# Kernel optimization log

Measured on AMD Instinct MI355X. Metric: run time of the kernel, lower is better.

## Reference

```python
import jax, jax.numpy as jnp
import numpy as np

L = 2048          # seq len
DIM = 1024        # model dim
NL = 12           # num layers
VOCAB = 50257
PAD_VOCAB = 50264 # vocab padded to multiple of 8 for embedding
N = 16            # ssm state dim
K = 4             # conv kernel size
E = 2048          # d_inner = expand * dim
DTR = 64          # dt_rank = ceil(dim/16)
EPS = 1e-5


def setup_inputs() -> dict:
    key = jax.random.key(0)
    ks = jax.random.split(key, 12)
    s = 0.02
    f32 = jnp.float32
    # HiPPO-style A init: A_log = log(1..N) broadcast over channels
    A_log = jnp.log(jnp.broadcast_to(jnp.arange(1, N + 1, dtype=f32), (NL, E, N)))
    return {
        "input_ids": jax.random.randint(ks[0], (L,), 0, VOCAB),
        "embed": jax.random.normal(ks[1], (PAD_VOCAB, DIM), f32) * s,
        "in_proj_w": jax.random.normal(ks[2], (NL, 2 * E, DIM), f32) * s,
        "conv_w": jax.random.normal(ks[3], (NL, E, K), f32) * s,
        "conv_b": jnp.zeros((NL, E), f32),
        "x_proj_w": jax.random.normal(ks[4], (NL, DTR + 2 * N, E), f32) * s,
        "dt_proj_w": jax.random.normal(ks[5], (NL, E, DTR), f32) * s,
        "dt_proj_b": jax.random.normal(ks[6], (NL, E), f32) * 0.1,
        "A_log": A_log,
        "D_param": jnp.ones((NL, E), f32),
        "out_proj_w": jax.random.normal(ks[7], (NL, DIM, E), f32) * s,
        "norm_w": jnp.ones((NL, DIM), f32),
        "norm_f_w": jnp.ones((DIM,), f32),
        "head_w": jax.random.normal(ks[8], (VOCAB, DIM), f32) * s,
    }


def rmsnorm(x, w):
    # per-token RMSNorm over last axis (matches eqx.nn.RMSNorm vmapped per token)
    inv = jax.lax.rsqrt(jnp.mean(x * x, axis=-1, keepdims=True) + EPS)
    return x * inv * w


def causal_dw_conv(x, w, b):
    # x: [L, E], w: [E, K] depthwise causal conv, b: [E]
    out = jax.lax.conv_general_dilated(
        x.T[None],            # [1, E, L]
        w[:, None, :],        # [E, 1, K]
        (1,), [(K - 1, 0)],
        feature_group_count=E,
        dimension_numbers=("NCH", "OIH", "NCH"),
    )
    return out[0].T + b       # [L, E]


def mamba_block(x, in_w, cw, cb, xp_w, dt_w, dt_b, A_log, D, out_w):
    # x: [L, DIM]
    xz = x @ in_w.T                       # [L, 2E]
    xi, z = xz[:, :E], xz[:, E:]
    xc = jax.nn.silu(causal_dw_conv(xi, cw, cb))   # [L, E]
    dbc = xc @ xp_w.T                     # [L, DTR + 2N]
    dt = jax.nn.softplus(dbc[:, :DTR] @ dt_w.T + dt_b)  # [L, E]
    B = dbc[:, DTR:DTR + N]               # [L, N]
    C = dbc[:, DTR + N:]                  # [L, N]
    A = -jnp.exp(A_log)                   # [E, N]
    dA = jnp.exp(dt[:, :, None] * A)                       # [L, E, N]
    dBu = dt[:, :, None] * B[:, None, :] * xc[:, :, None]  # [L, E, N]

    def step(h, inp):
        dA_t, dBu_t = inp
        h = dA_t * h + dBu_t
        return h, h

    _, hs = jax.lax.scan(step, jnp.zeros((E, N), x.dtype), (dA, dBu))
    y = jnp.einsum("len,ln->le", hs, C) + D * xc
    y = y * jax.nn.silu(z)
    return y @ out_w.T                    # [L, DIM]


def reference(input_ids, embed, in_proj_w, conv_w, conv_b, x_proj_w,
              dt_proj_w, dt_proj_b, A_log, D_param, out_proj_w,
              norm_w, norm_f_w, head_w):
    x = embed[input_ids]                  # [L, DIM]
    res = None
    for i in range(NL):
        res = x + res if res is not None else x
        h = rmsnorm(res, norm_w[i])
        x = mamba_block(h, in_proj_w[i], conv_w[i], conv_b[i], x_proj_w[i],
                        dt_proj_w[i], dt_proj_b[i], A_log[i], D_param[i],
                        out_proj_w[i])
    res = x + res
    x = rmsnorm(res, norm_f_w)
    return x @ head_w.T                   # [L, VOCAB]
```

## Files before the change

### kernel.cpp

```cpp
#include <hip/hip_runtime.h>
#include <math.h>

#define LSEQ 2048
#define DMODEL 1024
#define NLAYER 12
#define NVOCAB 50257
#define NPADV 50304
#define EDIM 2048
#define NST 16
#define DTRANK 64
#define EPSV 1e-5f
#define NCHUNK 64
#define TCHUNK 32

typedef __attribute__((ext_vector_type(4))) float float4v;
typedef __attribute__((ext_vector_type(8))) short short8v;
typedef __attribute__((ext_vector_type(4))) unsigned short ushort4v;
typedef unsigned short u16;

__device__ __forceinline__ u16 f2bf(float f) {
    union { float f; unsigned int u; } v; v.f = f;
    unsigned int r = v.u + 0x7FFFu + ((v.u >> 16) & 1u);
    return (u16)(r >> 16);
}

__device__ __forceinline__ ushort4v cvt4(float4 a) {
    ushort4v r; r[0] = f2bf(a.x); r[1] = f2bf(a.y); r[2] = f2bf(a.z); r[3] = f2bf(a.w);
    return r;
}

__device__ __forceinline__ float4v mfma_bf16(short8v a, short8v b, float4v c) {
    return __builtin_amdgcn_mfma_f32_16x16x32_bf16(a, b, c, 0, 0, 0);
}

__device__ __forceinline__ void gload_lds16(const void* g, void* l) {
    __builtin_amdgcn_global_load_lds(
        (const __attribute__((address_space(1))) unsigned int*)g,
        (__attribute__((address_space(3))) unsigned int*)l,
        16, 0, 0);
}

__global__ __launch_bounds__(256) void k_embed(const int* __restrict__ ids,
                                               const float* __restrict__ emb,
                                               float* __restrict__ res) {
    const int t = blockIdx.x;
    const int row = ids[t];
    ((float4*)(res + (size_t)t * DMODEL))[threadIdx.x] =
        ((const float4*)(emb + (size_t)row * DMODEL))[threadIdx.x];
}

template<bool ADD>
__global__ __launch_bounds__(256) void k_addnorm(float* __restrict__ res,
                                                 const float* __restrict__ xin,
                                                 const float* __restrict__ w,
                                                 u16* __restrict__ h) {
    const int t = blockIdx.x;
    const int i = threadIdx.x;
    float4 r = ((float4*)(res + (size_t)t * DMODEL))[i];
    if (ADD) {
        float4 xv = ((const float4*)(xin + (size_t)t * DMODEL))[i];
        r.x += xv.x; r.y += xv.y; r.z += xv.z; r.w += xv.w;
        ((float4*)(res + (size_t)t * DMODEL))[i] = r;
    }
    float ss = r.x * r.x + r.y * r.y + r.z * r.z + r.w * r.w;
#pragma unroll
    for (int off = 32; off > 0; off >>= 1) ss += __shfl_xor(ss, off);
    __shared__ float part[4];
    if ((i & 63) == 0) part[i >> 6] = ss;
    __syncthreads();
    float tot = part[0] + part[1] + part[2] + part[3];
    const float inv = rsqrtf(tot * (1.f / DMODEL) + EPSV);
    float4 wv = ((const float4*)w)[i];
    float4 o;
    o.x = r.x * inv * wv.x; o.y = r.y * inv * wv.y;
    o.z = r.z * inv * wv.z; o.w = r.w * inv * wv.w;
    ((ushort4v*)(h + (size_t)t * DMODEL))[i] = cvt4(o);
}

__global__ __launch_bounds__(256) void k_cvt(const float* __restrict__ s, u16* __restrict__ d,
                                             long long n, long long ntot) {
    const long long stride = (long long)gridDim.x * 256 * 8;
    for (long long i = ((long long)blockIdx.x * 256 + threadIdx.x) * 8; i < ntot; i += stride) {
        ushort4v lo, hi;
        if (i < n) {
            float4 a = *(const float4*)(s + i);
            float4 b = *(const float4*)(s + i + 4);
            lo = cvt4(a); hi = cvt4(b);
        } else {
            lo[0] = lo[1] = lo[2] = lo[3] = 0;
            hi[0] = hi[1] = hi[2] = hi[3] = 0;
        }
        *(ushort4v*)(d + i) = lo;
        *(ushort4v*)(d + i + 4) = hi;
    }
}

__global__ __launch_bounds__(256) void k_cvtL(const float* __restrict__ sa, u16* __restrict__ da, long long na,
                                              const float* __restrict__ sb, u16* __restrict__ db, long long nb,
                                              const float* __restrict__ sc, u16* __restrict__ dc, long long nc,
                                              const float* __restrict__ sd, u16* __restrict__ dd, long long nd) {
    const long long tot = na + nb + nc + nd;
    const long long stride = (long long)gridDim.x * 256 * 8;
    for (long long i = ((long long)blockIdx.x * 256 + threadIdx.x) * 8; i < tot; i += stride) {
        const float* s; u16* d; long long o = i;
        if (o < na) { s = sa; d = da; }
        else { o -= na;
            if (o < nb) { s = sb; d = db; }
            else { o -= nb;
                if (o < nc) { s = sc; d = dc; }
                else { o -= nc; s = sd; d = dd; } } }
        float4 a = *(const float4*)(s + o);
        float4 b = *(const float4*)(s + o + 4);
        *(ushort4v*)(d + o) = cvt4(a);
        *(ushort4v*)(d + o + 4) = cvt4(b);
    }
}

template<int MT, int EPI, bool NTS>
__global__ __launch_bounds__(256, 3) void k_gemm128(const u16* __restrict__ A,
                                                    const u16* __restrict__ W,
                                                    float* __restrict__ C,
                                                    const float* __restrict__ bias,
                                                    int N, int K, int ldc, int cpx) {
    __shared__ __align__(128) u16 lds[3][8192];
    const int tid = threadIdx.x;
    const int w = tid >> 6;
    const int lane = tid & 63;
    const int l16 = lane & 15;
    const int quad = lane >> 4;
    const int wm = (w >> 1) * 64;
    const int wn = (w & 1) * 64;
    const int bid = blockIdx.x;
    const int orig = (bid & 7) * cpx + (bid >> 3);
    const int bm = orig & (MT - 1);
    const int bn = orig / MT;
    const int row0 = bm * 128, col0 = bn * 128;

    const int scol = ((lane & 3) ^ ((lane >> 3) & 3)) * 8;
    const int lrow = lane >> 2;
    const u16* sbase[4];
#pragma unroll
    for (int c = 0; c < 4; ++c) {
        const int g = w * 4 + c;
        sbase[c] = (g < 8 ? A + (size_t)(row0 + g * 16 + lrow) * K
                          : W + (size_t)(col0 + (g - 8) * 16 + lrow) * K) + scol;
    }

    const int swz = (quad ^ ((l16 >> 1) & 3)) * 8;
    const int aoff = (wm + l16) * 32 + swz;
    const int boff = 4096 + (wn + l16) * 32 + swz;

    float4v acc[4][4];
#pragma unroll
    for (int i = 0; i < 4; ++i)
#pragma unroll
        for (int j = 0; j < 4; ++j)
#pragma unroll
            for (int r = 0; r < 4; ++r) acc[i][j][r] = 0.f;

    const int NT = K >> 5;
    u16* lds0 = &lds[0][0];

    auto stage_tile = [&](int buf, int t) {
        u16* dst = lds0 + buf * 8192;
#pragma unroll
        for (int c = 0; c < 4; ++c)
            gload_lds16(sbase[c] + t * 32, dst + (w * 4 + c) * 512);
    };

    stage_tile(0, 0);
    stage_tile(1, 1);
    asm volatile("s_waitcnt vmcnt(4)" ::: "memory");
    __builtin_amdgcn_s_barrier();

    int cur = 0;
    for (int n = 0; n < NT; ++n) {
        const u16* Ls = lds0 + cur * 8192;
        short8v af[4], bf[4];
#pragma unroll
        for (int ii = 0; ii < 4; ++ii)
            af[ii] = *(const short8v*)&Ls[aoff + ii * 512];
#pragma unroll
        for (int j = 0; j < 4; ++j)
            bf[j] = *(const short8v*)&Ls[boff + j * 512];
        const bool pf = (n + 2 < NT);
        if (pf) {
            int tg = cur + 2; if (tg >= 3) tg -= 3;
            stage_tile(tg, n + 2);
        }
        __builtin_amdgcn_s_setprio(1);
#pragma unroll
        for (int ii = 0; ii < 4; ++ii)
#pragma unroll
            for (int j = 0; j < 4; ++j)
                acc[ii][j] = mfma_bf16(af[ii], bf[j], acc[ii][j]);
        __builtin_amdgcn_s_setprio(0);
        if (pf)
            asm volatile("s_waitcnt vmcnt(4)" ::: "memory");
        else if (n + 1 < NT)
            asm volatile("s_waitcnt vmcnt(0)" ::: "memory");
        __builtin_amdgcn_s_barrier();
        ++cur; if (cur == 3) cur = 0;
    }

    float* lt = (float*)lds0 + (size_t)w * 1040;
    const int ecol = col0 + wn + lane;
    float bv = 0.f;
    if (EPI == 1) bv = bias[(ecol < N) ? ecol : 0];
#pragma unroll
    for (int i = 0; i < 4; ++i) {
        __syncthreads();
#pragma unroll
        for (int j = 0; j < 4; ++j)
#pragma unroll
            for (int r = 0; r < 4; ++r)
                lt[(quad * 4 + r) * 65 + j * 16 + l16] = acc[i][j][r];
        __syncthreads();
        if (ecol < N) {
            const int rbase = row0 + wm + i * 16;
#pragma unroll
            for (int t = 0; t < 16; ++t) {
                float v = lt[t * 65 + lane];
                if (EPI == 1) { v += bv; v = (v > 20.f) ? v : log1pf(__expf(v)); }
                float* p = &C[(size_t)(rbase + t) * ldc + ecol];
                if (NTS) __builtin_nontemporal_store(v, p);
                else *p = v;
            }
        }
    }
}

template<int MT>
__global__ __launch_bounds__(256, 3) void k_gemm64(const u16* __restrict__ A,
                                                   const u16* __restrict__ W,
                                                   float* __restrict__ C,
                                                   int N, int K, int ldc, int cpx) {
    __shared__ __align__(128) u16 lds[3][8192];
    const int tid = threadIdx.x;
    const int w = tid >> 6;
    const int lane = tid & 63;
    const int l16 = lane & 15;
    const int quad = lane >> 4;
    const int wm = (w >> 1) * 32;
    const int wn = (w & 1) * 32;
    const int bid = blockIdx.x;
    const int orig = (bid & 7) * cpx + (bid >> 3);
    const int bm = orig & (MT - 1);
    const int bn = orig / MT;
    const int row0 = bm * 64, col0 = bn * 64;

    const int scol = ((lane & 3) ^ ((lane >> 3) & 3)) * 8;
    const int lrow = lane >> 2;
    const u16* sbase[4];
#pragma unroll
    for (int c = 0; c < 4; ++c) {
        const int ch = w * 4 + c;
        const int isA = (ch < 8);
        const int cc = isA ? ch : (ch - 8);
        const int half = cc >> 2;
        const int rbase = (cc & 3) * 16;
        sbase[c] = (isA ? A + (size_t)(row0 + rbase + lrow) * K
                        : W + (size_t)(col0 + rbase + lrow) * K) + half * 32 + scol;
    }

    const int swz = (quad ^ ((l16 >> 1) & 3)) * 8;
    const int aoff = (wm + l16) * 32 + swz;
    const int boff = 4096 + (wn + l16) * 32 + swz;

    float4v acc[2][2];
#pragma unroll
    for (int i = 0; i < 2; ++i)
#pragma unroll
        for (int j = 0; j < 2; ++j)
#pragma unroll
            for (int r = 0; r < 4; ++r) acc[i][j][r] = 0.f;

    const int NT = K >> 6;
    u16* lds0 = &lds[0][0];

    auto stage_tile = [&](int buf, int t) {
        u16* dst = lds0 + buf * 8192;
#pragma unroll
        for (int c = 0; c < 4; ++c)
            gload_lds16(sbase[c] + t * 64, dst + (w * 4 + c) * 512);
    };

    stage_tile(0, 0);
    stage_tile(1, 1);
    asm volatile("s_waitcnt vmcnt(4)" ::: "memory");
    __builtin_amdgcn_s_barrier();

    int cur = 0;
    for (int n = 0; n < NT; ++n) {
        const u16* Ls = lds0 + cur * 8192;
        short8v af[2][2], bf[2][2];
#pragma unroll
        for (int ks = 0; ks < 2; ++ks) {
#pragma unroll
            for (int ii = 0; ii < 2; ++ii)
                af[ks][ii] = *(const short8v*)&Ls[ks * 2048 + aoff + ii * 512];
#pragma unroll
            for (int j = 0; j < 2; ++j)
                bf[ks][j] = *(const short8v*)&Ls[ks * 2048 + boff + j * 512];
        }
        const bool pf = (n + 2 < NT);
        if (pf) {
            int tg = cur + 2; if (tg >= 3) tg -= 3;
            stage_tile(tg, n + 2);
        }
        __builtin_amdgcn_s_setprio(1);
#pragma unroll
        for (int ks = 0; ks < 2; ++ks)
#pragma unroll
            for (int ii = 0; ii < 2; ++ii)
#pragma unroll
                for (int j = 0; j < 2; ++j)
                    acc[ii][j] = mfma_bf16(af[ks][ii], bf[ks][j], acc[ii][j]);
        __builtin_amdgcn_s_setprio(0);
        if (pf)
            asm volatile("s_waitcnt vmcnt(4)" ::: "memory");
        else if (n + 1 < NT)
            asm volatile("s_waitcnt vmcnt(0)" ::: "memory");
        __builtin_amdgcn_s_barrier();
        ++cur; if (cur == 3) cur = 0;
    }

    float* lt = (float*)lds0 + (size_t)w * 528;
    const int c32 = lane & 31;
    const int rsub = lane >> 5;
    const int ecol = col0 + wn + c32;
#pragma unroll
    for (int i = 0; i < 2; ++i) {
        __syncthreads();
#pragma unroll
        for (int j = 0; j < 2; ++j)
#pragma unroll
            for (int r = 0; r < 4; ++r)
                lt[(quad * 4 + r) * 33 + j * 16 + l16] = acc[i][j][r];
        __syncthreads();
        if (ecol < N) {
            const int rbase = row0 + wm + i * 16;
#pragma unroll
            for (int t = 0; t < 8; ++t)
                C[(size_t)(rbase + 2 * t + rsub) * ldc + ecol] =
                    lt[(2 * t + rsub) * 33 + c32];
        }
    }
}

__global__ __launch_bounds__(256) void k_conv(const float* __restrict__ xz,
                                              const float* __restrict__ cw,
                                              const float* __restrict__ cb,
                                              float* __restrict__ xc,
                                              u16* __restrict__ xc16) {
    const int e = blockIdx.x * 256 + threadIdx.x;
    const int t0 = blockIdx.y * 8;
    const float w0 = cw[e * 4 + 0], w1 = cw[e * 4 + 1], w2 = cw[e * 4 + 2], w3 = cw[e * 4 + 3];
    const float b = cb[e];
    float xm3 = (t0 >= 3) ? xz[(size_t)(t0 - 3) * (2 * EDIM) + e] : 0.f;
    float xm2 = (t0 >= 2) ? xz[(size_t)(t0 - 2) * (2 * EDIM) + e] : 0.f;
    float xm1 = (t0 >= 1) ? xz[(size_t)(t0 - 1) * (2 * EDIM) + e] : 0.f;
#pragma unroll
    for (int s = 0; s < 8; ++s) {
        const int t = t0 + s;
        const float xt = xz[(size_t)t * (2 * EDIM) + e];
        const float v = w0 * xm3 + w1 * xm2 + w2 * xm1 + w3 * xt + b;
        const float sv = v / (1.f + __expf(-v));
        xc[(size_t)t * EDIM + e] = sv;
        xc16[(size_t)t * EDIM + e] = f2bf(sv);
        xm3 = xm2; xm2 = xm1; xm1 = xt;
    }
}

__global__ __launch_bounds__(256) void k_xproj(const u16* __restrict__ xc,
                                               const u16* __restrict__ W,
                                               float* __restrict__ dbc,
                                               u16* __restrict__ dbc16) {
    const int tid = threadIdx.x;
    const int wave = tid >> 6, lane = tid & 63;
    const int l16 = lane & 15, quad = lane >> 4;
    const int m = blockIdx.x * 16 + l16;
    const int kb = wave * (EDIM / 4);
    float4v acc[6];
#pragma unroll
    for (int j = 0; j < 6; ++j)
#pragma unroll
        for (int r = 0; r < 4; ++r) acc[j][r] = 0.f;

    for (int ks = 0; ks < EDIM / 4; ks += 32) {
        const int k = kb + ks + quad * 8;
        const short8v af = *(const short8v*)(xc + (size_t)m * EDIM + k);
#pragma unroll
        for (int j = 0; j < 6; ++j) {
            const short8v bf = *(const short8v*)(W + (size_t)(j * 16 + l16) * EDIM + k);
            acc[j] = mfma_bf16(af, bf, acc[j]);
        }
    }
    __shared__ float red[4][16][96];
#pragma unroll
    for (int j = 0; j < 6; ++j)
#pragma unroll
        for (int r = 0; r < 4; ++r)
            red[wave][quad * 4 + r][j * 16 + l16] = acc[j][r];
    __syncthreads();
    for (int idx = tid; idx < 16 * 96; idx += 256) {
        const int r = idx / 96, c = idx % 96;
        const float s = red[0][r][c] + red[1][r][c] + red[2][r][c] + red[3][r][c];
        const int row = blockIdx.x * 16 + r;
        dbc[(size_t)row * 96 + c] = s;
        if (c < 64) dbc16[(size_t)row * 64 + c] = f2bf(s);
    }
}

__global__ __launch_bounds__(256) void k_scanA(const float* __restrict__ dt,
                                               const float* __restrict__ xc,
                                               const float* __restrict__ dbc,
                                               const float* __restrict__ Al,
                                               float* __restrict__ hpart,
                                               float* __restrict__ sdtb) {
    const int e = blockIdx.y * 256 + threadIdx.x;
    const int c = blockIdx.x;
    float a[NST];
#pragma unroll
    for (int n = 0; n < NST; ++n) a[n] = -__expf(Al[(size_t)e * NST + n]);
    bool fast = true;
#pragma unroll
    for (int n = 0; n < NST; ++n)
        fast = fast && (fabsf(a[n] + (float)(n + 1)) < 1e-3f * (float)(n + 1));
    __align__(16) float h[NST];
#pragma unroll
    for (int n = 0; n < NST; ++n) h[n] = 0.f;
    float sdt = 0.f;
    const int t0 = c * TCHUNK;
    if (fast) {
        for (int s = 0; s < TCHUNK; ++s) {
            const int t = t0 + s;
            const float d = dt[(size_t)t * EDIM + e];
            const float x = xc[(size_t)t * EDIM + e];
            __align__(16) float Bv[NST];
#pragma unroll
            for (int q = 0; q < 4; ++q)
                *(float4*)&Bv[q * 4] = *(const float4*)&dbc[(size_t)t * 96 + 64 + q * 4];
            const float u = d * x;
            sdt += d;
            const float d1 = __expf(-d);
            float pw = 1.f;
#pragma unroll
            for (int n = 0; n < NST; ++n) { pw *= d1; h[n] = fmaf(pw, h[n], u * Bv[n]); }
        }
    } else {
        for (int s = 0; s < TCHUNK; ++s) {
            const int t = t0 + s;
            const float d = dt[(size_t)t * EDIM + e];
            const float x = xc[(size_t)t * EDIM + e];
            __align__(16) float Bv[NST];
#pragma unroll
            for (int q = 0; q < 4; ++q)
                *(float4*)&Bv[q * 4] = *(const float4*)&dbc[(size_t)t * 96 + 64 + q * 4];
            const float u = d * x;
            sdt += d;
#pragma unroll
            for (int n = 0; n < NST; ++n) h[n] = fmaf(__expf(d * a[n]), h[n], u * Bv[n]);
        }
    }
#pragma unroll
    for (int n = 0; n < NST; n += 4)
        *(float4*)&hpart[((size_t)c * EDIM + e) * NST + n] = *(float4*)&h[n];
    sdtb[(size_t)c * EDIM + e] = sdt;
}

__global__ __launch_bounds__(256) void k_scanB(float* __restrict__ hio,
                                               const float* __restrict__ sdtb,
                                               const float* __restrict__ Al) {
    const int idx = blockIdx.x * 256 + threadIdx.x;
    const int e = idx >> 4;
    const float a = -__expf(Al[idx]);
    float carry = 0.f;
    for (int c = 0; c < NCHUNK; ++c) {
        const size_t off = ((size_t)c * EDIM + e) * NST + (idx & 15);
        const float hp = hio[off];
        const float ap = __expf(a * sdtb[(size_t)c * EDIM + e]);
        hio[off] = carry;
        carry = fmaf(ap, carry, hp);
    }
}

__global__ __launch_bounds__(256) void k_scanC(const float* __restrict__ dt,
                                               const float* __restrict__ xc,
                                               const float* __restrict__ dbc,
                                               const float* __restrict__ xz,
                                               const float* __restrict__ Al,
                                               const float* __restrict__ Dl,
                                               const float* __restrict__ hin,
                                               u16* __restrict__ y) {
    const int e = blockIdx.y * 256 + threadIdx.x;
    const int c = blockIdx.x;
    float a[NST];
#pragma unroll
    for (int n = 0; n < NST; ++n) a[n] = -__expf(Al[(size_t)e * NST + n]);
    bool fast = true;
#pragma unroll
    for (int n = 0; n < NST; ++n)
        fast = fast && (fabsf(a[n] + (float)(n + 1)) < 1e-3f * (float)(n + 1));
    __align__(16) float h[NST];
#pragma unroll
    for (int n = 0; n < NST; n += 4)
        *(float4*)&h[n] = *(const float4*)&hin[((size_t)c * EDIM + e) * NST + n];
    const float Dv = Dl[e];
    const int t0 = c * TCHUNK;
    for (int s = 0; s < TCHUNK; ++s) {
        const int t = t0 + s;
        const float d = dt[(size_t)t * EDIM + e];
        const float x = xc[(size_t)t * EDIM + e];
        __align__(16) float Bv[NST], Cv[NST];
#pragma unroll
        for (int q = 0; q < 4; ++q) {
            *(float4*)&Bv[q * 4] = *(const float4*)&dbc[(size_t)t * 96 + 64 + q * 4];
            *(float4*)&Cv[q * 4] = *(const float4*)&dbc[(size_t)t * 96 + 80 + q * 4];
        }
        const float u = d * x;
        float ys = 0.f;
        if (fast) {
            const float d1 = __expf(-d);
            float pw = 1.f;
#pragma unroll
            for (int n = 0; n < NST; ++n) {
                pw *= d1;
                h[n] = fmaf(pw, h[n], u * Bv[n]);
                ys = fmaf(h[n], Cv[n], ys);
            }
        } else {
#pragma unroll
            for (int n = 0; n < NST; ++n) {
                h[n] = fmaf(__expf(d * a[n]), h[n], u * Bv[n]);
                ys = fmaf(h[n], Cv[n], ys);
            }
        }
        const float z = xz[(size_t)t * (2 * EDIM) + EDIM + e];
        const float yv = ys + Dv * x;
        y[(size_t)t * EDIM + e] = f2bf(yv * (z / (1.f + __expf(-z))));
    }
}

extern "C" void kernel_launch(void* const* d_in, const int* in_sizes, int n_in,
                              void* d_out, int out_size, void* d_ws, size_t ws_size,
                              hipStream_t stream) {
    const int*   ids   = (const int*)d_in[0];
    const float* emb   = (const float*)d_in[1];
    const float* inW   = (const float*)d_in[2];
    const float* convW = (const float*)d_in[3];
    const float* convB = (const float*)d_in[4];
    const float* xpW   = (const float*)d_in[5];
    const float* dtW   = (const float*)d_in[6];
    const float* dtB   = (const float*)d_in[7];
    const float* Alog  = (const float*)d_in[8];
    const float* Dpar  = (const float*)d_in[9];
    const float* outW  = (const float*)d_in[10];
    const float* normW = (const float*)d_in[11];
    const float* normF = (const float*)d_in[12];
    const float* headW = (const float*)d_in[13];
    float* out = (float*)d_out;

    float* ws    = (float*)d_ws;
    float* res   = ws;
    float* xzb   = res   + (size_t)LSEQ * DMODEL;
    float* xcb   = xzb   + (size_t)LSEQ * 2 * EDIM;
    float* dbcb  = xcb   + (size_t)LSEQ * EDIM;
    float* dtb   = dbcb  + (size_t)LSEQ * 96;
    float* xob   = dtb   + (size_t)LSEQ * EDIM;
    float* hpart = xob   + (size_t)LSEQ * DMODEL;
    float* sdtb  = hpart + (size_t)NCHUNK * EDIM * NST;
    u16* hbf  = (u16*)(sdtb + (size_t)NCHUNK * EDIM);
    u16* ybf  = hbf  + (size_t)LSEQ * DMODEL;
    u16* wbf  = ybf  + (size_t)LSEQ * EDIM;
    u16* wbf2 = wbf  + (size_t)2 * EDIM * DMODEL;
    u16* xc16  = wbf  + (size_t)12 * 1024 * 1024;
    u16* dbc16 = xc16 + (size_t)LSEQ * EDIM;
    u16* xpw16 = dbc16 + (size_t)LSEQ * DTRANK;
    u16* dtw16 = xpw16 + (size_t)96 * EDIM;

    k_embed<<<LSEQ, 256, 0, stream>>>(ids, emb, res);

    for (int i = 0; i < NLAYER; ++i) {
        if (i == 0)
            k_addnorm<false><<<LSEQ, 256, 0, stream>>>(res, nullptr, normW, hbf);
        else
            k_addnorm<true><<<LSEQ, 256, 0, stream>>>(res, xob, normW + (size_t)i * DMODEL, hbf);

        k_cvtL<<<4096, 256, 0, stream>>>(
            inW  + (size_t)i * 2 * EDIM * DMODEL, wbf,   (long long)2 * EDIM * DMODEL,
            outW + (size_t)i * DMODEL * EDIM,     wbf2,  (long long)DMODEL * EDIM,
            xpW  + (size_t)i * 96 * EDIM,         xpw16, (long long)96 * EDIM,
            dtW  + (size_t)i * EDIM * DTRANK,     dtw16, (long long)EDIM * DTRANK);

        k_gemm128<16, 0, false><<<dim3(512), 256, 0, stream>>>(hbf, wbf, xzb, nullptr,
                2 * EDIM, DMODEL, 2 * EDIM, 64);

        k_conv<<<dim3(8, 256), 256, 0, stream>>>(xzb, convW + (size_t)i * EDIM * 4,
                convB + (size_t)i * EDIM, xcb, xc16);

        k_xproj<<<128, 256, 0, stream>>>(xc16, xpw16, dbcb, dbc16);

        k_gemm128<16, 1, false><<<dim3(256), 256, 0, stream>>>(dbc16, dtw16, dtb,
                dtB + (size_t)i * EDIM, EDIM, DTRANK, EDIM, 32);

        const float* Al = Alog + (size_t)i * EDIM * NST;
        k_scanA<<<dim3(NCHUNK, EDIM / 256), 256, 0, stream>>>(dtb, xcb, dbcb, Al, hpart, sdtb);
        k_scanB<<<(EDIM * NST) / 256, 256, 0, stream>>>(hpart, sdtb, Al);
        k_scanC<<<dim3(NCHUNK, EDIM / 256), 256, 0, stream>>>(dtb, xcb, dbcb, xzb, Al,
                Dpar + (size_t)i * EDIM, hpart, ybf);

        k_gemm64<32><<<dim3(512), 256, 0, stream>>>(ybf, wbf2, xob,
                DMODEL, EDIM, DMODEL, 64);
    }

    k_addnorm<true><<<LSEQ, 256, 0, stream>>>(res, xob, normF, hbf);

    k_cvt<<<4096, 256, 0, stream>>>(headW, wbf,
            (long long)NVOCAB * DMODEL, (long long)NPADV * DMODEL);
    k_gemm128<16, 0, true><<<dim3(6288), 256, 0, stream>>>(hbf, wbf, out, nullptr,
            NVOCAB, DMODEL, NVOCAB, 6288 / 8);
}
```

Baseline: 2.883 ms.

## Batch all-layer weight conversion, double-buffer head GEMM, widen epilogue stores

When the workspace is large enough, all per-layer weights are converted to bf16 in a single launch up front, replacing twelve separate conversion kernels. The head GEMM gets a two-buffer LDS variant with a higher occupancy bound. The GEMM epilogue is also rewritten to stage a full 128-column tile in LDS, so each row is written with 128 contiguous floats rather than 64. The tradeoffs are a larger workspace requirement, which falls back to per-layer conversion when it is not met, and an extra barrier per K step in the two-buffer loop.

```diff
diff --git a/kernel.cpp b/kernel.cpp
--- a/kernel.cpp
+++ b/kernel.cpp
@@ -116,13 +116,14 @@
     }
 }
 
-template<int MT, int EPI, bool NTS>
-__global__ __launch_bounds__(256, 3) void k_gemm128(const u16* __restrict__ A,
-                                                    const u16* __restrict__ W,
-                                                    float* __restrict__ C,
-                                                    const float* __restrict__ bias,
-                                                    int N, int K, int ldc, int cpx) {
-    __shared__ __align__(128) u16 lds[3][8192];
+template<int MT, int EPI, bool NTS, int NBUF>
+__global__ __launch_bounds__(256, NBUF == 2 ? 4 : 3)
+void k_gemm128(const u16* __restrict__ A,
+               const u16* __restrict__ W,
+               float* __restrict__ C,
+               const float* __restrict__ bias,
+               int N, int K, int ldc, int cpx) {
+    __shared__ __align__(128) u16 lds[NBUF][8192];
     const int tid = threadIdx.x;
     const int w = tid >> 6;
     const int lane = tid & 63;
@@ -173,58 +174,91 @@
     asm volatile("s_waitcnt vmcnt(4)" ::: "memory");
     __builtin_amdgcn_s_barrier();
 
-    int cur = 0;
-    for (int n = 0; n < NT; ++n) {
-        const u16* Ls = lds0 + cur * 8192;
-        short8v af[4], bf[4];
-#pragma unroll
-        for (int ii = 0; ii < 4; ++ii)
-            af[ii] = *(const short8v*)&Ls[aoff + ii * 512];
-#pragma unroll
-        for (int j = 0; j < 4; ++j)
-            bf[j] = *(const short8v*)&Ls[boff + j * 512];
-        const bool pf = (n + 2 < NT);
-        if (pf) {
-            int tg = cur + 2; if (tg >= 3) tg -= 3;
-            stage_tile(tg, n + 2);
-        }
-        __builtin_amdgcn_s_setprio(1);
-#pragma unroll
-        for (int ii = 0; ii < 4; ++ii)
+    if constexpr (NBUF == 2) {
+        for (int n = 0; n < NT; ++n) {
+            const u16* Ls = lds0 + (n & 1) * 8192;
+            short8v af[4], bf[4];
+#pragma unroll
+            for (int ii = 0; ii < 4; ++ii)
+                af[ii] = *(const short8v*)&Ls[aoff + ii * 512];
 #pragma unroll
             for (int j = 0; j < 4; ++j)
-                acc[ii][j] = mfma_bf16(af[ii], bf[j], acc[ii][j]);
-        __builtin_amdgcn_s_setprio(0);
-        if (pf)
-            asm volatile("s_waitcnt vmcnt(4)" ::: "memory");
-        else if (n + 1 < NT)
-            asm volatile("s_waitcnt vmcnt(0)" ::: "memory");
-        __builtin_amdgcn_s_barrier();
-        ++cur; if (cur == 3) cur = 0;
-    }
-
-    float* lt = (float*)lds0 + (size_t)w * 1040;
-    const int ecol = col0 + wn + lane;
+                bf[j] = *(const short8v*)&Ls[boff + j * 512];
+            __builtin_amdgcn_s_barrier();
+            __builtin_amdgcn_s_setprio(1);
+#pragma unroll
+            for (int ii = 0; ii < 4; ++ii)
+#pragma unroll
+                for (int j = 0; j < 4; ++j)
+                    acc[ii][j] = mfma_bf16(af[ii], bf[j], acc[ii][j]);
+            __builtin_amdgcn_s_setprio(0);
+            if (n + 2 < NT) {
+                stage_tile(n & 1, n + 2);
+                asm volatile("s_waitcnt vmcnt(4)" ::: "memory");
+            } else if (n < NT - 1) {
+                asm volatile("s_waitcnt vmcnt(0)" ::: "memory");
+            }
+            __builtin_amdgcn_s_barrier();
+        }
+    } else {
+        int cur = 0;
+        for (int n = 0; n < NT; ++n) {
+            const u16* Ls = lds0 + cur * 8192;
+            short8v af[4], bf[4];
+#pragma unroll
+            for (int ii = 0; ii < 4; ++ii)
+                af[ii] = *(const short8v*)&Ls[aoff + ii * 512];
+#pragma unroll
+            for (int j = 0; j < 4; ++j)
+                bf[j] = *(const short8v*)&Ls[boff + j * 512];
+            const bool pf = (n + 2 < NT);
+            if (pf) {
+                int tg = cur + 2; if (tg >= 3) tg -= 3;
+                stage_tile(tg, n + 2);
+            }
+            __builtin_amdgcn_s_setprio(1);
+#pragma unroll
+            for (int ii = 0; ii < 4; ++ii)
+#pragma unroll
+                for (int j = 0; j < 4; ++j)
+                    acc[ii][j] = mfma_bf16(af[ii], bf[j], acc[ii][j]);
+            __builtin_amdgcn_s_setprio(0);
+            if (pf)
+                asm volatile("s_waitcnt vmcnt(4)" ::: "memory");
+            else if (n + 1 < NT)
+                asm volatile("s_waitcnt vmcnt(0)" ::: "memory");
+            __builtin_amdgcn_s_barrier();
+            ++cur; if (cur == 3) cur = 0;
+        }
+    }
+
+    float* lt = (float*)lds0;
+    const int ecol = col0 + (tid & 127);
+    const int rsel = tid >> 7;
     float bv = 0.f;
-    if (EPI == 1) bv = bias[(ecol < N) ? ecol : 0];
-#pragma unroll
-    for (int i = 0; i < 4; ++i) {
+    if (EPI == 1 && ecol < N) bv = bias[ecol];
+#pragma unroll
+    for (int g = 0; g < 8; ++g) {
         __syncthreads();
-#pragma unroll
-        for (int j = 0; j < 4; ++j)
-#pragma unroll
-            for (int r = 0; r < 4; ++r)
-                lt[(quad * 4 + r) * 65 + j * 16 + l16] = acc[i][j][r];
+        if ((w >> 1) == (g >> 2)) {
+            const int ii = g & 3;
+#pragma unroll
+            for (int j = 0; j < 4; ++j)
+#pragma unroll
+                for (int r = 0; r < 4; ++r)
+                    lt[(quad * 4 + r) * 132 + wn + j * 16 + l16] = acc[ii][j][r];
+        }
         __syncthreads();
         if (ecol < N) {
-            const int rbase = row0 + wm + i * 16;
-#pragma unroll
-            for (int t = 0; t < 16; ++t) {
-                float v = lt[t * 65 + lane];
+            const int rbase = row0 + g * 16;
+#pragma unroll
+            for (int p = 0; p < 8; ++p) {
+                const int rr = p * 2 + rsel;
+                float v = lt[rr * 132 + (tid & 127)];
                 if (EPI == 1) { v += bv; v = (v > 20.f) ? v : log1pf(__expf(v)); }
-                float* p = &C[(size_t)(rbase + t) * ldc + ecol];
-                if (NTS) __builtin_nontemporal_store(v, p);
-                else *p = v;
+                float* pp = &C[(size_t)(rbase + rr) * ldc + ecol];
+                if (NTS) __builtin_nontemporal_store(v, pp);
+                else *pp = v;
             }
         }
     }
@@ -579,7 +613,22 @@
     u16* xpw16 = dbc16 + (size_t)LSEQ * DTRANK;
     u16* dtw16 = xpw16 + (size_t)96 * EDIM;
 
+    const long long nInAll  = (long long)NLAYER * 2 * EDIM * DMODEL;
+    const long long nOutAll = (long long)NLAYER * DMODEL * EDIM;
+    const long long nXpAll  = (long long)NLAYER * 96 * EDIM;
+    const long long nDtAll  = (long long)NLAYER * EDIM * DTRANK;
+    u16* wAllIn  = wbf + (size_t)NPADV * DMODEL;
+    u16* wAllOut = wAllIn  + nInAll;
+    u16* wAllXp  = wAllOut + nOutAll;
+    u16* wAllDt  = wAllXp  + nXpAll;
+    const size_t need = (size_t)((char*)(wAllDt + nDtAll) - (char*)d_ws);
+    const bool oneshot = (ws_size >= need);
+
     k_embed<<<LSEQ, 256, 0, stream>>>(ids, emb, res);
+
+    if (oneshot)
+        k_cvtL<<<8192, 256, 0, stream>>>(inW, wAllIn, nInAll, outW, wAllOut, nOutAll,
+                                         xpW, wAllXp, nXpAll, dtW, wAllDt, nDtAll);
 
     for (int i = 0; i < NLAYER; ++i) {
         if (i == 0)
@@ -587,21 +636,30 @@
         else
             k_addnorm<true><<<LSEQ, 256, 0, stream>>>(res, xob, normW + (size_t)i * DMODEL, hbf);
 
-        k_cvtL<<<4096, 256, 0, stream>>>(
-            inW  + (size_t)i * 2 * EDIM * DMODEL, wbf,   (long long)2 * EDIM * DMODEL,
-            outW + (size_t)i * DMODEL * EDIM,     wbf2,  (long long)DMODEL * EDIM,
-            xpW  + (size_t)i * 96 * EDIM,         xpw16, (long long)96 * EDIM,
-            dtW  + (size_t)i * EDIM * DTRANK,     dtw16, (long long)EDIM * DTRANK);
-
-        k_gemm128<16, 0, false><<<dim3(512), 256, 0, stream>>>(hbf, wbf, xzb, nullptr,
+        const u16 *wIn, *wOut, *wXp, *wDt;
+        if (oneshot) {
+            wIn  = wAllIn  + (size_t)i * 2 * EDIM * DMODEL;
+            wOut = wAllOut + (size_t)i * DMODEL * EDIM;
+            wXp  = wAllXp  + (size_t)i * 96 * EDIM;
+            wDt  = wAllDt  + (size_t)i * EDIM * DTRANK;
+        } else {
+            k_cvtL<<<4096, 256, 0, stream>>>(
+                inW  + (size_t)i * 2 * EDIM * DMODEL, wbf,   (long long)2 * EDIM * DMODEL,
+                outW + (size_t)i * DMODEL * EDIM,     wbf2,  (long long)DMODEL * EDIM,
+                xpW  + (size_t)i * 96 * EDIM,         xpw16, (long long)96 * EDIM,
+                dtW  + (size_t)i * EDIM * DTRANK,     dtw16, (long long)EDIM * DTRANK);
+            wIn = wbf; wOut = wbf2; wXp = xpw16; wDt = dtw16;
+        }
+
+        k_gemm128<16, 0, false, 3><<<dim3(512), 256, 0, stream>>>(hbf, wIn, xzb, nullptr,
                 2 * EDIM, DMODEL, 2 * EDIM, 64);
 
         k_conv<<<dim3(8, 256), 256, 0, stream>>>(xzb, convW + (size_t)i * EDIM * 4,
                 convB + (size_t)i * EDIM, xcb, xc16);
 
-        k_xproj<<<128, 256, 0, stream>>>(xc16, xpw16, dbcb, dbc16);
-
-        k_gemm128<16, 1, false><<<dim3(256), 256, 0, stream>>>(dbc16, dtw16, dtb,
+        k_xproj<<<128, 256, 0, stream>>>(xc16, wXp, dbcb, dbc16);
+
+        k_gemm128<16, 1, false, 3><<<dim3(256), 256, 0, stream>>>(dbc16, wDt, dtb,
                 dtB + (size_t)i * EDIM, EDIM, DTRANK, EDIM, 32);
 
         const float* Al = Alog + (size_t)i * EDIM * NST;
@@ -610,7 +668,7 @@
         k_scanC<<<dim3(NCHUNK, EDIM / 256), 256, 0, stream>>>(dtb, xcb, dbcb, xzb, Al,
                 Dpar + (size_t)i * EDIM, hpart, ybf);
 
-        k_gemm64<32><<<dim3(512), 256, 0, stream>>>(ybf, wbf2, xob,
+        k_gemm64<32><<<dim3(512), 256, 0, stream>>>(ybf, wOut, xob,
                 DMODEL, EDIM, DMODEL, 64);
     }
 
@@ -618,6 +676,6 @@
 
     k_cvt<<<4096, 256, 0, stream>>>(headW, wbf,
             (long long)NVOCAB * DMODEL, (long long)NPADV * DMODEL);
-    k_gemm128<16, 0, true><<<dim3(6288), 256, 0, stream>>>(hbf, wbf, out, nullptr,
+    k_gemm128<16, 0, true, 2><<<dim3(6288), 256, 0, stream>>>(hbf, wbf, out, nullptr,
             NVOCAB, DMODEL, NVOCAB, 6288 / 8);
 }
```

Measured after the change: 3.005 ms. +4.2%, slower.
